# Performance work log

Measured on AMD Instinct MI355X. Metric: run time of the kernel, lower is better.

The kernel has to match this reference:

```python
import jax, jax.numpy as jnp
import numpy as np

B, S, D, H = 4, 2048, 1024, 16
DK = D // H


def setup_inputs() -> dict:
    key = jax.random.key(0)
    ks = jax.random.split(key, 12)
    s = 1.0 / np.sqrt(D)
    inp = {
        "query": jax.random.normal(ks[0], (B, S, D), jnp.float32),
        "key": jax.random.normal(ks[1], (B, S, D), jnp.float32),
        "value": jax.random.normal(ks[2], (B, S, D), jnp.float32),
        "mask": jax.random.randint(ks[3], (B, S, S), 0, 2, jnp.int32),
        "Wq": jax.random.uniform(ks[4], (D, D), jnp.float32, -s, s),
        "bq": jax.random.uniform(ks[5], (D,), jnp.float32, -s, s),
        "Wk": jax.random.uniform(ks[6], (D, D), jnp.float32, -s, s),
        "bk": jax.random.uniform(ks[7], (D,), jnp.float32, -s, s),
        "Wv": jax.random.uniform(ks[8], (D, D), jnp.float32, -s, s),
        "bv": jax.random.uniform(ks[9], (D,), jnp.float32, -s, s),
        "Wo": jax.random.uniform(ks[10], (D, D), jnp.float32, -s, s),
        "bo": jax.random.uniform(ks[11], (D,), jnp.float32, -s, s),
    }
    return inp


def reference(query, key, value, mask, Wq, bq, Wk, bk, Wv, bv, Wo, bo):
    # Linear projections (torch Linear: x @ W.T + b), split into heads: [B,H,S,DK]
    def proj(x, W, b):
        y = x @ W.T + b
        return y.reshape(B, S, H, DK).transpose(0, 2, 1, 3)

    q = proj(query, Wq, bq)
    k = proj(key, Wk, bk)
    v = proj(value, Wv, bv)

    # scores: [B,H,S,S]
    scores = jnp.einsum("bhqd,bhkd->bhqk", q, k) / jnp.sqrt(jnp.float32(DK))
    m = mask[:, None, :, :]  # broadcast over heads
    scores = jnp.where(m == 0, jnp.float32(-1e9), scores)
    attn = jax.nn.softmax(scores, axis=-1)
    out = jnp.einsum("bhqk,bhkd->bhqd", attn, v)
    out = out.transpose(0, 2, 1, 3).reshape(B, S, D)
    return out @ Wo.T + bo
```

## Files before the change

### kernel.cpp

```cpp
#include <hip/hip_runtime.h>

#define B_  4
#define S_  2048
#define D_  1024
#define H_  16
#define DK_ 64

typedef __attribute__((ext_vector_type(8))) __bf16 bf16x8;
typedef __attribute__((ext_vector_type(4))) float  f32x4;

#define AS1 __attribute__((address_space(1)))
#define AS3 __attribute__((address_space(3)))

__device__ __forceinline__ void gl2lds16(const void* g, void* l) {
    __builtin_amdgcn_global_load_lds((const AS1 unsigned int*)g,
                                     (AS3 unsigned int*)l, 16, 0, 0);
}

__device__ __forceinline__ unsigned short f2bf(float f) {
    union { float f; unsigned u; } v; v.f = f;
    return (unsigned short)((v.u + 0x7FFFu + ((v.u >> 16) & 1u)) >> 16);
}

__device__ __forceinline__ unsigned cvt_pk_bf16(float lo, float hi) {
    unsigned r;
    asm("v_cvt_pk_bf16_f32 %0, %1, %2" : "=v"(r) : "v"(lo), "v"(hi));
    return r;
}

__device__ __forceinline__ void cast8(const float* __restrict__ x,
                                      unsigned short* __restrict__ y, int i) {
    float4 a = ((const float4*)x)[2 * i];
    float4 b = ((const float4*)x)[2 * i + 1];
    uint4 w;
    w.x = cvt_pk_bf16(a.x, a.y);
    w.y = cvt_pk_bf16(a.z, a.w);
    w.z = cvt_pk_bf16(b.x, b.y);
    w.w = cvt_pk_bf16(b.z, b.w);
    ((uint4*)y)[i] = w;
}

__global__ __launch_bounds__(256) void prep_all(
    const float* __restrict__ q, const float* __restrict__ k,
    const float* __restrict__ v, const float* __restrict__ Wq,
    const float* __restrict__ Wk, const float* __restrict__ Wv,
    const float* __restrict__ Wo, const int* __restrict__ mask,
    unsigned short* __restrict__ qb, unsigned short* __restrict__ kb,
    unsigned short* __restrict__ vb, unsigned short* __restrict__ wqb,
    unsigned short* __restrict__ wkb, unsigned short* __restrict__ wvb,
    unsigned short* __restrict__ wob, unsigned long long* __restrict__ pmo)
{
    const int bid = blockIdx.x;
    if (bid < 12288) {
        const int sel = bid >> 12;
        const float* x = (sel == 0) ? q : (sel == 1) ? k : v;
        unsigned short* y = (sel == 0) ? qb : (sel == 1) ? kb : vb;
        cast8(x, y, (bid & 4095) * 256 + threadIdx.x);
    } else if (bid < 14336) {
        const int b2 = bid - 12288;
        const int sel = b2 >> 9;
        const float* x = (sel == 0) ? Wq : (sel == 1) ? Wk : (sel == 2) ? Wv : Wo;
        unsigned short* y = (sel == 0) ? wqb : (sel == 1) ? wkb : (sel == 2) ? wvb : wob;
        cast8(x, y, (b2 & 511) * 256 + threadIdx.x);
    } else {
        const int b3 = bid - 14336;
        const int lane = threadIdx.x & 63;
        int w = (b3 * 256 + (int)threadIdx.x) >> 6;
        #pragma unroll 4
        for (int it = 0; it < 32; ++it, w += 8192) {
            const int mv = mask[(size_t)w * 64 + lane];
            const unsigned long long bal = __ballot(mv != 0);
            if (lane == 0) pmo[w] = bal;
        }
    }
}

__global__ __launch_bounds__(256, 3) void gemm_qkv(
    const unsigned short* __restrict__ Xq, const unsigned short* __restrict__ Xk,
    const unsigned short* __restrict__ Xv, const unsigned short* __restrict__ Wqkv,
    const float* __restrict__ bq, const float* __restrict__ bk,
    const float* __restrict__ bv, unsigned short* __restrict__ Qw,
    unsigned short* __restrict__ Kw, unsigned short* __restrict__ Vt,
    float qscale)
{
    __shared__ unsigned short As[128 * 64];
    __shared__ unsigned short Bs[128 * 64];

    const int tid  = threadIdx.x;
    const int lane = tid & 63, wave = tid >> 6;
    const int l16  = lane & 15, quad = lane >> 4;
    const int wm = wave & 1, wn = wave >> 1;

    const int lin = blockIdx.y * 24 + blockIdx.x;
    const int xcd = lin & 7;
    const int i   = lin >> 3;
    const int ng  = i >> 5;
    const int r_  = i & 31;
    const int bx  = ng * 4 + (r_ & 3);
    const int by  = xcd * 8 + (r_ >> 2);

    const int n0 = bx * 128, m0 = by * 128;
    const int xr = l16 & 7;

    const int sel = bx >> 3;
    const unsigned short* X = (sel == 0) ? Xq : (sel == 1) ? Xk : Xv;

    const int row8 = lane >> 3;
    const int sc   = ((lane & 7) ^ row8) * 8;

    f32x4 acc[4][4] = {};

    for (int k0 = 0; k0 < D_; k0 += 64) {
        __syncthreads();
        #pragma unroll
        for (int j = 0; j < 4; ++j) {
            const int ca = wave * 4 + j;
            const int r  = ca * 8 + row8;
            gl2lds16(X    + (size_t)(m0 + r) * D_ + k0 + sc, &As[ca * 512 + (lane & 63) * 8]);
            gl2lds16(Wqkv + (size_t)(n0 + r) * D_ + k0 + sc, &Bs[ca * 512 + (lane & 63) * 8]);
        }
        __syncthreads();

        #pragma unroll
        for (int s = 0; s < 2; ++s) {
            bf16x8 a[4], bb[4];
            #pragma unroll
            for (int i2 = 0; i2 < 4; ++i2)
                a[i2] = *(const bf16x8*)&As[(wm * 64 + i2 * 16 + l16) * 64 + (((s * 4 + quad) ^ xr)) * 8];
            #pragma unroll
            for (int j = 0; j < 4; ++j)
                bb[j] = *(const bf16x8*)&Bs[(wn * 64 + j * 16 + l16) * 64 + (((s * 4 + quad) ^ xr)) * 8];
            #pragma unroll
            for (int i2 = 0; i2 < 4; ++i2)
                #pragma unroll
                for (int j = 0; j < 4; ++j)
                    acc[i2][j] = __builtin_amdgcn_mfma_f32_16x16x32_bf16(a[i2], bb[j], acc[i2][j], 0, 0, 0);
        }
    }

    const int ncol = (bx & 7) * 128 + wn * 64;
    const float scale = (sel == 0) ? qscale : 1.0f;
    const float* bias = (sel == 0) ? bq : (sel == 1) ? bk : bv;

    if (sel == 2) {
        const int bb_ = m0 >> 11;
        #pragma unroll
        for (int j = 0; j < 4; ++j) {
            const int dk = ncol + j * 16 + l16;
            const float bvv = bias[dk];
            #pragma unroll
            for (int i2 = 0; i2 < 4; ++i2) {
                const int sb = (m0 & (S_ - 1)) + wm * 64 + i2 * 16 + quad * 4;
                uint2 w;
                w.x = cvt_pk_bf16(acc[i2][j][0] + bvv, acc[i2][j][1] + bvv);
                w.y = cvt_pk_bf16(acc[i2][j][2] + bvv, acc[i2][j][3] + bvv);
                *(uint2*)(Vt + (size_t)(bb_ * D_ + dk) * S_ + sb) = w;
            }
        }
    } else {
        unsigned short* Outp = sel ? Kw : Qw;
        #pragma unroll
        for (int j = 0; j < 4; ++j) {
            const int n = ncol + j * 16 + l16;
            const float bvv = bias[n];
            #pragma unroll
            for (int i2 = 0; i2 < 4; ++i2) {
                #pragma unroll
                for (int r = 0; r < 4; ++r) {
                    const int m = m0 + wm * 64 + i2 * 16 + quad * 4 + r;
                    Outp[(size_t)m * D_ + n] = f2bf((acc[i2][j][r] + bvv) * scale);
                }
            }
        }
    }
}

__global__ __launch_bounds__(256, 4) void gemm_out(
    const unsigned short* __restrict__ X, const unsigned short* __restrict__ W,
    const float* __restrict__ bias, float* __restrict__ Out)
{
    __shared__ unsigned short As[128 * 64];
    __shared__ unsigned short Bs[64 * 64];

    const int tid  = threadIdx.x;
    const int lane = tid & 63, wave = tid >> 6;
    const int l16  = lane & 15, quad = lane >> 4;
    const int wm = wave & 1, wn = wave >> 1;

    const int lin = blockIdx.y * 16 + blockIdx.x;
    const int xcd = lin & 7;
    const int i   = lin >> 3;
    const int ng  = i >> 5;
    const int r_  = i & 31;
    const int bx  = ng * 4 + (r_ & 3);
    const int by  = xcd * 8 + (r_ >> 2);

    const int n0 = bx * 64, m0 = by * 128;
    const int xr = l16 & 7;

    const int row8 = lane >> 3;
    const int sc   = ((lane & 7) ^ row8) * 8;

    f32x4 acc[4][2] = {};

    for (int k0 = 0; k0 < D_; k0 += 64) {
        __syncthreads();
        #pragma unroll
        for (int j = 0; j < 4; ++j) {
            const int ca = wave * 4 + j;
            const int r  = ca * 8 + row8;
            gl2lds16(X + (size_t)(m0 + r) * D_ + k0 + sc, &As[ca * 512 + (lane & 63) * 8]);
        }
        #pragma unroll
        for (int j = 0; j < 2; ++j) {
            const int c = j * 256 + tid;
            const int row = c >> 3;
            const int cl = (c & 7) ^ (row & 7);
            gl2lds16(W + (size_t)(n0 + row) * D_ + k0 + cl * 8, &Bs[c * 8]);
        }
        __syncthreads();

        #pragma unroll
        for (int s = 0; s < 2; ++s) {
            bf16x8 a[4], bb[2];
            #pragma unroll
            for (int i2 = 0; i2 < 4; ++i2)
                a[i2] = *(const bf16x8*)&As[(wm * 64 + i2 * 16 + l16) * 64 + (((s * 4 + quad) ^ xr)) * 8];
            #pragma unroll
            for (int j = 0; j < 2; ++j)
                bb[j] = *(const bf16x8*)&Bs[(wn * 32 + j * 16 + l16) * 64 + (((s * 4 + quad) ^ xr)) * 8];
            #pragma unroll
            for (int i2 = 0; i2 < 4; ++i2)
                #pragma unroll
                for (int j = 0; j < 2; ++j)
                    acc[i2][j] = __builtin_amdgcn_mfma_f32_16x16x32_bf16(a[i2], bb[j], acc[i2][j], 0, 0, 0);
        }
    }

    #pragma unroll
    for (int j = 0; j < 2; ++j) {
        const int n = n0 + wn * 32 + j * 16 + l16;
        const float bv = bias[n];
        #pragma unroll
        for (int i2 = 0; i2 < 4; ++i2) {
            #pragma unroll
            for (int r = 0; r < 4; ++r) {
                const int m = m0 + wm * 64 + i2 * 16 + quad * 4 + r;
                Out[(size_t)m * D_ + n] = acc[i2][j][r] + bv;
            }
        }
    }
}

__global__ __launch_bounds__(256, 4) void attn_kernel(
    const unsigned short* __restrict__ Q,
    const unsigned short* __restrict__ Kg,
    const unsigned short* __restrict__ Vt,
    const unsigned long long* __restrict__ pm,
    unsigned short* __restrict__ O)
{
    __shared__ unsigned short Ks[64 * 64];
    __shared__ unsigned short Vs[2][64 * 64];
    __shared__ unsigned short Ps[128 * 64];

    const int tid  = threadIdx.x;
    const int lane = tid & 63, wave = tid >> 6;
    const int l16  = lane & 15, quad = lane >> 4;

    const int n  = blockIdx.y * 16 + blockIdx.x;
    const int ns = (n & 7) * 128 + (n >> 3);
    const int b  = ns >> 8;
    const int h  = (ns >> 4) & 15;
    const int q0 = (ns & 15) * 128;
    const int xq = l16 & 7;

    union { uint4 u; bf16x8 v; } ones_u;
    ones_u.u = make_uint4(0x3F803F80u, 0x3F803F80u, 0x3F803F80u, 0x3F803F80u);
    const bf16x8 vb_ones = ones_u.v;

    bf16x8 qa[2][2];
    #pragma unroll
    for (int qf = 0; qf < 2; ++qf) {
        const unsigned short* qp =
            Q + (size_t)(b * S_ + q0 + wave * 32 + qf * 16 + l16) * D_ + h * DK_ + quad * 8;
        qa[qf][0] = *(const bf16x8*)qp;
        qa[qf][1] = *(const bf16x8*)(qp + 32);
    }

    const unsigned short* Kbase = Kg + (size_t)(b * S_) * D_ + h * DK_;
    const unsigned short* Vbase = Vt + (size_t)(b * D_ + h * DK_) * S_;

    auto stageK = [&](int kt2) {
        const int k0 = kt2 * 64;
        #pragma unroll
        for (int j = 0; j < 2; ++j) {
            const int c = j * 256 + tid;
            const int row = c >> 3;
            const int cl = (c & 7) ^ (row & 7);
            gl2lds16(Kbase + (size_t)(k0 + row) * D_ + cl * 8, &Ks[c * 8]);
        }
    };
    auto stageV = [&](int bi2, int kt2) {
        const int k0 = kt2 * 64;
        #pragma unroll
        for (int j = 0; j < 2; ++j) {
            const int c = j * 256 + tid;
            const int row = c >> 3;
            const int cl = (c & 7) ^ (row & 7);
            gl2lds16(Vbase + (size_t)row * S_ + k0 + cl * 8, &Vs[bi2][c * 8]);
        }
    };

    const unsigned long long* pmq0 =
        pm + (size_t)(b * S_ + q0 + wave * 32 + l16) * (S_ / 64);
    const unsigned long long* pmq1 = pmq0 + (size_t)16 * (S_ / 64);

    f32x4 oacc[2][5] = {};

    stageK(0);
    stageV(0, 0);
    __syncthreads();

    int bi = 0;
    for (int kt = 0; kt < S_ / 64; ++kt) {
        const bool more = (kt + 1 < S_ / 64);
        const unsigned long long wq0 = pmq0[kt];
        const unsigned long long wq1 = pmq1[kt];
        if (more) stageV(bi ^ 1, kt + 1);

        #pragma unroll
        for (int half = 0; half < 2; ++half) {
            f32x4 sct[2][2] = {};
            __builtin_amdgcn_s_setprio(1);
            #pragma unroll
            for (int s = 0; s < 2; ++s) {
                const int cs = ((s * 4 + quad) ^ xq) * 8;
                #pragma unroll
                for (int mbh = 0; mbh < 2; ++mbh) {
                    bf16x8 ka = *(const bf16x8*)&Ks[((half * 2 + mbh) * 16 + l16) * 64 + cs];
                    sct[mbh][0] = __builtin_amdgcn_mfma_f32_16x16x32_bf16(ka, qa[0][s], sct[mbh][0], 0, 0, 0);
                    sct[mbh][1] = __builtin_amdgcn_mfma_f32_16x16x32_bf16(ka, qa[1][s], sct[mbh][1], 0, 0, 0);
                }
            }
            __builtin_amdgcn_s_setprio(0);

            #pragma unroll
            for (int qf = 0; qf < 2; ++qf) {
                const unsigned long long wq = qf ? wq1 : wq0;
                #pragma unroll
                for (int mbh = 0; mbh < 2; ++mbh) {
                    const int mb = half * 2 + mbh;
                    const unsigned nib = (unsigned)(wq >> (mb * 16 + quad * 4)) & 0xFu;
                    float e[4];
                    #pragma unroll
                    for (int r = 0; r < 4; ++r) {
                        float x = __builtin_amdgcn_exp2f(sct[mbh][qf][r]);
                        e[r] = ((nib >> r) & 1u) ? x : 0.f;
                    }
                    uint2 w;
                    w.x = cvt_pk_bf16(e[0], e[1]);
                    w.y = cvt_pk_bf16(e[2], e[3]);
                    *(uint2*)&Ps[(wave * 32 + qf * 16 + l16) * 64 +
                                 ((mb * 16 + quad * 4) ^ (xq * 8))] = w;
                }
            }
        }

        __syncthreads();
        if (more) stageK(kt + 1);

        __builtin_amdgcn_s_setprio(1);
        #pragma unroll
        for (int s = 0; s < 2; ++s) {
            const int cs = ((s * 4 + quad) ^ xq) * 8;
            bf16x8 pa0 = *(const bf16x8*)&Ps[(wave * 32 + l16) * 64 +
                                             ((s * 32 + quad * 8) ^ (xq * 8))];
            bf16x8 pa1 = *(const bf16x8*)&Ps[(wave * 32 + 16 + l16) * 64 +
                                             ((s * 32 + quad * 8) ^ (xq * 8))];
            #pragma unroll
            for (int db = 0; db < 4; ++db) {
                bf16x8 vb = *(const bf16x8*)&Vs[bi][(db * 16 + l16) * 64 + cs];
                oacc[0][db] = __builtin_amdgcn_mfma_f32_16x16x32_bf16(pa0, vb, oacc[0][db], 0, 0, 0);
                oacc[1][db] = __builtin_amdgcn_mfma_f32_16x16x32_bf16(pa1, vb, oacc[1][db], 0, 0, 0);
            }
            oacc[0][4] = __builtin_amdgcn_mfma_f32_16x16x32_bf16(pa0, vb_ones, oacc[0][4], 0, 0, 0);
            oacc[1][4] = __builtin_amdgcn_mfma_f32_16x16x32_bf16(pa1, vb_ones, oacc[1][4], 0, 0, 0);
        }
        __builtin_amdgcn_s_setprio(0);

        __syncthreads();
        bi ^= 1;
    }

    #pragma unroll
    for (int qf = 0; qf < 2; ++qf) {
        #pragma unroll
        for (int r = 0; r < 4; ++r) {
            const float linv = 1.0f / oacc[qf][4][r];
            const int qg = q0 + wave * 32 + qf * 16 + quad * 4 + r;
            #pragma unroll
            for (int db = 0; db < 4; ++db) {
                O[(size_t)(b * S_ + qg) * D_ + h * DK_ + db * 16 + l16] =
                    f2bf(oacc[qf][db][r] * linv);
            }
        }
    }
}

extern "C" void kernel_launch(void* const* d_in, const int* in_sizes, int n_in,
                              void* d_out, int out_size, void* d_ws, size_t ws_size,
                              hipStream_t stream)
{
    const float* q   = (const float*)d_in[0];
    const float* k   = (const float*)d_in[1];
    const float* v   = (const float*)d_in[2];
    const int* mask  = (const int*)d_in[3];
    const float* Wq  = (const float*)d_in[4];
    const float* bq  = (const float*)d_in[5];
    const float* Wk  = (const float*)d_in[6];
    const float* bk  = (const float*)d_in[7];
    const float* Wv  = (const float*)d_in[8];
    const float* bv  = (const float*)d_in[9];
    const float* Wo  = (const float*)d_in[10];
    const float* bo  = (const float*)d_in[11];

    const size_t MN = (size_t)B_ * S_ * D_;
    const size_t WN = (size_t)D_ * D_;
    unsigned short* qb  = (unsigned short*)d_ws;
    unsigned short* kb  = qb + MN;
    unsigned short* vb  = kb + MN;
    unsigned short* Qw  = vb + MN;
    unsigned short* Kw  = Qw + MN;
    unsigned short* Vt  = Kw + MN;
    unsigned short* wqb = Vt + MN;
    unsigned short* wkb = wqb + WN;
    unsigned short* wvb = wkb + WN;
    unsigned short* wob = wvb + WN;
    unsigned short* Ow  = qb;
    unsigned long long* pm = (unsigned long long*)d_out;

    dim3 blk(256);

    prep_all<<<dim3(16384), blk, 0, stream>>>(
        q, k, v, Wq, Wk, Wv, Wo, mask,
        qb, kb, vb, wqb, wkb, wvb, wob, pm);

    const float qscale = 1.44269504088896341f * 0.125f;

    gemm_qkv<<<dim3(3 * D_ / 128, (B_ * S_) / 128), blk, 0, stream>>>(
        qb, kb, vb, wqb, bq, bk, bv, Qw, Kw, Vt, qscale);

    attn_kernel<<<dim3(S_ / 128, B_ * H_), blk, 0, stream>>>(Qw, Kw, Vt, pm, Ow);

    gemm_out<<<dim3(D_ / 64, (B_ * S_) / 128), blk, 0, stream>>>(
        Ow, wob, bo, (float*)d_out);
}
```

Measured before the change: 379.5 us.

## Fuse activation fp32-to-bf16 cast into QKV GEMM A-tile loads

```diff
diff --git a/kernel.cpp b/kernel.cpp
--- a/kernel.cpp
+++ b/kernel.cpp
@@ -41,29 +41,21 @@
 }
 
 __global__ __launch_bounds__(256) void prep_all(
-    const float* __restrict__ q, const float* __restrict__ k,
-    const float* __restrict__ v, const float* __restrict__ Wq,
-    const float* __restrict__ Wk, const float* __restrict__ Wv,
-    const float* __restrict__ Wo, const int* __restrict__ mask,
-    unsigned short* __restrict__ qb, unsigned short* __restrict__ kb,
-    unsigned short* __restrict__ vb, unsigned short* __restrict__ wqb,
-    unsigned short* __restrict__ wkb, unsigned short* __restrict__ wvb,
-    unsigned short* __restrict__ wob, unsigned long long* __restrict__ pmo)
+    const float* __restrict__ Wq, const float* __restrict__ Wk,
+    const float* __restrict__ Wv, const float* __restrict__ Wo,
+    const int* __restrict__ mask,
+    unsigned short* __restrict__ wqb, unsigned short* __restrict__ wkb,
+    unsigned short* __restrict__ wvb, unsigned short* __restrict__ wob,
+    unsigned long long* __restrict__ pmo)
 {
     const int bid = blockIdx.x;
-    if (bid < 12288) {
-        const int sel = bid >> 12;
-        const float* x = (sel == 0) ? q : (sel == 1) ? k : v;
-        unsigned short* y = (sel == 0) ? qb : (sel == 1) ? kb : vb;
-        cast8(x, y, (bid & 4095) * 256 + threadIdx.x);
-    } else if (bid < 14336) {
-        const int b2 = bid - 12288;
-        const int sel = b2 >> 9;
+    if (bid < 2048) {
+        const int sel = bid >> 9;
         const float* x = (sel == 0) ? Wq : (sel == 1) ? Wk : (sel == 2) ? Wv : Wo;
         unsigned short* y = (sel == 0) ? wqb : (sel == 1) ? wkb : (sel == 2) ? wvb : wob;
-        cast8(x, y, (b2 & 511) * 256 + threadIdx.x);
+        cast8(x, y, (bid & 511) * 256 + threadIdx.x);
     } else {
-        const int b3 = bid - 14336;
+        const int b3 = bid - 2048;
         const int lane = threadIdx.x & 63;
         int w = (b3 * 256 + (int)threadIdx.x) >> 6;
         #pragma unroll 4
@@ -76,8 +68,8 @@
 }
 
 __global__ __launch_bounds__(256, 3) void gemm_qkv(
-    const unsigned short* __restrict__ Xq, const unsigned short* __restrict__ Xk,
-    const unsigned short* __restrict__ Xv, const unsigned short* __restrict__ Wqkv,
+    const float* __restrict__ Xq, const float* __restrict__ Xk,
+    const float* __restrict__ Xv, const unsigned short* __restrict__ Wqkv,
     const float* __restrict__ bq, const float* __restrict__ bk,
     const float* __restrict__ bv, unsigned short* __restrict__ Qw,
     unsigned short* __restrict__ Kw, unsigned short* __restrict__ Vt,
@@ -103,23 +95,42 @@
     const int xr = l16 & 7;
 
     const int sel = bx >> 3;
-    const unsigned short* X = (sel == 0) ? Xq : (sel == 1) ? Xk : Xv;
+    const float* X = (sel == 0) ? Xq : (sel == 1) ? Xk : Xv;
 
     const int row8 = lane >> 3;
     const int sc   = ((lane & 7) ^ row8) * 8;
 
+    uint4 apf[4];
+    auto loadA = [&](int k0) {
+        #pragma unroll
+        for (int j = 0; j < 4; ++j) {
+            const int r = (wave * 4 + j) * 8 + row8;
+            const float4* ap =
+                (const float4*)(X + (size_t)(m0 + r) * D_ + k0 + sc);
+            float4 lo = ap[0], hi = ap[1];
+            uint4 w;
+            w.x = cvt_pk_bf16(lo.x, lo.y);
+            w.y = cvt_pk_bf16(lo.z, lo.w);
+            w.z = cvt_pk_bf16(hi.x, hi.y);
+            w.w = cvt_pk_bf16(hi.z, hi.w);
+            apf[j] = w;
+        }
+    };
+
     f32x4 acc[4][4] = {};
 
+    loadA(0);
     for (int k0 = 0; k0 < D_; k0 += 64) {
         __syncthreads();
         #pragma unroll
         for (int j = 0; j < 4; ++j) {
             const int ca = wave * 4 + j;
             const int r  = ca * 8 + row8;
-            gl2lds16(X    + (size_t)(m0 + r) * D_ + k0 + sc, &As[ca * 512 + (lane & 63) * 8]);
             gl2lds16(Wqkv + (size_t)(n0 + r) * D_ + k0 + sc, &Bs[ca * 512 + (lane & 63) * 8]);
-        }
-        __syncthreads();
+            *(uint4*)&As[ca * 512 + (lane & 63) * 8] = apf[j];
+        }
+        __syncthreads();
+        if (k0 + 64 < D_) loadA(k0 + 64);
 
         #pragma unroll
         for (int s = 0; s < 2; ++s) {
@@ -441,14 +452,13 @@
 
     dim3 blk(256);
 
-    prep_all<<<dim3(16384), blk, 0, stream>>>(
-        q, k, v, Wq, Wk, Wv, Wo, mask,
-        qb, kb, vb, wqb, wkb, wvb, wob, pm);
+    prep_all<<<dim3(4096), blk, 0, stream>>>(
+        Wq, Wk, Wv, Wo, mask, wqb, wkb, wvb, wob, pm);
 
     const float qscale = 1.44269504088896341f * 0.125f;
 
     gemm_qkv<<<dim3(3 * D_ / 128, (B_ * S_) / 128), blk, 0, stream>>>(
-        qb, kb, vb, wqb, bq, bk, bv, Qw, Kw, Vt, qscale);
+        q, k, v, wqb, bq, bk, bv, Qw, Kw, Vt, qscale);
 
     attn_kernel<<<dim3(S_ / 128, B_ * H_), blk, 0, stream>>>(Qw, Kw, Vt, pm, Ow);
 
```

Result: slower. 412.2 us (+8.6%).
